# Kernel optimization log

Hardware: AMD Instinct MI355X
Metric: run time of the kernel (lower is better)

The kernel has to match this reference:

```python
import jax, jax.numpy as jnp
import numpy as np

B, C_IN, T = 8, 1024, 4096
VQ_C, CODEBOOK, DS = 1024, 2048, 2


def setup_inputs() -> dict:
    key = jax.random.key(0)
    ks = jax.random.split(key, 6)
    return {
        "x": jax.random.normal(ks[0], (B, C_IN, T), jnp.float32),
        "x_mask": jnp.ones((B, 1, T), jnp.float32),
        "w_in": jax.random.normal(ks[1], (VQ_C, C_IN, DS), jnp.float32) * 0.02,
        "b_in": jnp.zeros((VQ_C,), jnp.float32),
        "embed": jax.random.normal(ks[2], (CODEBOOK, VQ_C), jnp.float32),
        "w_out": jax.random.normal(ks[3], (C_IN, VQ_C), jnp.float32) * 0.02,
        "b_out": jnp.zeros((C_IN,), jnp.float32),
    }


def reference(x, x_mask, w_in, b_in, embed, w_out, b_out):
    x_len = x.shape[2]
    ds = w_in.shape[-1]
    pad = (-x_len) % ds  # static under jit
    if pad:
        x = jnp.pad(x, ((0, 0), (0, 0), (0, pad)))
        x_mask = jnp.pad(x_mask, ((0, 0), (0, 0), (0, pad)))
    b, cin, tp = x.shape
    # conv_in: Conv1d(k=ds, stride=ds) == non-overlapping window contraction
    h = jnp.einsum('bcls,ocs->bol', x.reshape(b, cin, tp // ds, ds), w_in) + b_in[None, :, None]  # [B, D, L]
    tokens = h.transpose(0, 2, 1)  # [B, L, D]
    # euclidean codebook: ||t - e||^2 expanded (stable for argmin)
    d2 = (jnp.sum(tokens * tokens, -1, keepdims=True)
          - 2.0 * jnp.einsum('bld,nd->bln', tokens, embed)
          + jnp.sum(embed * embed, -1)[None, None, :])  # [B, L, N]
    idx = jnp.argmin(d2, axis=-1)  # [B, L]
    q = embed[idx]  # gather -> [B, L, D]
    # commitment loss (training-mode math; EMA codebook -> embed not a grad path)
    commit_loss = jnp.mean((jax.lax.stop_gradient(q) - tokens) ** 2)
    # straight-through estimator
    q_st = tokens + jax.lax.stop_gradient(q - tokens)
    q_cf = q_st.transpose(0, 2, 1)  # [B, D, L]
    # conv_out: nearest upsample x ds, then 1x1 conv
    up = jnp.repeat(q_cf, ds, axis=2)  # [B, D, Tp]
    out = jnp.einsum('bct,oc->bot', up, w_out) + b_out[None, :, None]
    out = out * x_mask
    return out[:, :, :x_len], commit_loss
```

## Files before the change

### kernel.cpp

```cpp
#include <hip/hip_runtime.h>

typedef _Float16 half8 __attribute__((ext_vector_type(8)));
typedef float f32x4 __attribute__((ext_vector_type(4)));

static constexpr int D = 1024;
static constexpr int NCODE = 2048;
static constexpr int MTOK = 16384;
static constexpr int KIN = 2048;
static constexpr int TLEN = 4096;
static constexpr int CAP = 2048;
#define TAU 0.4f

__device__ __forceinline__ void gload16(const void* g, void* l) {
  __builtin_amdgcn_global_load_lds(
      (const __attribute__((address_space(1))) void*)g,
      (__attribute__((address_space(3))) void*)l, 16, 0, 0);
}

#define SBAR()   asm volatile("s_barrier" ::: "memory")
#define WAITV4() asm volatile("s_waitcnt vmcnt(4)" ::: "memory")
#define WAITV0() asm volatile("s_waitcnt vmcnt(0)" ::: "memory")

__device__ __forceinline__ float key_to_f32(unsigned u) {
  unsigned bits = (u & 0x80000000u) ? (u & 0x7FFFFFFFu) : ~u;
  return __uint_as_float(bits);
}
__device__ __forceinline__ unsigned f32_to_key(float f) {
  unsigned ub = __float_as_uint(f);
  return (ub & 0x80000000u) ? ~ub : (ub | 0x80000000u);
}

__global__ __launch_bounds__(256) void k_pack_x(const float* __restrict__ x,
                                                _Float16* __restrict__ xh,
                                                _Float16* __restrict__ xl) {
  __shared__ float lds[32][65];
  const int tt0 = blockIdx.x * 64;
  const int cc0 = blockIdx.y * 32;
  const int b = blockIdx.z;
  const float* xb = x + ((size_t)b * D + cc0) * TLEN + tt0;
#pragma unroll
  for (int i = 0; i < 8; ++i) {
    int idx = threadIdx.x + i * 256;
    lds[idx >> 6][idx & 63] = xb[(size_t)(idx >> 6) * TLEN + (idx & 63)];
  }
  __syncthreads();
  const size_t mrow0 = (size_t)b * 2048 + (tt0 >> 1);
#pragma unroll
  for (int i = 0; i < 8; ++i) {
    int idx = threadIdx.x + i * 256;
    int r = idx >> 6, kk = idx & 63;
    float v = lds[kk >> 1][2 * r + (kk & 1)];
    _Float16 h = (_Float16)v;
    size_t off = (mrow0 + r) * (size_t)KIN + (size_t)cc0 * 2 + kk;
    xh[off] = h;
    xl[off] = (_Float16)(v - (float)h);
  }
}

__global__ __launch_bounds__(256) void k_split(const float* __restrict__ s,
                                               _Float16* __restrict__ hi,
                                               _Float16* __restrict__ lo, int n) {
  int i = blockIdx.x * 256 + threadIdx.x;
  if (i < n) {
    float v = s[i];
    _Float16 h = (_Float16)v;
    hi[i] = h;
    lo[i] = (_Float16)(v - (float)h);
  }
}

__global__ __launch_bounds__(256) void k_tohalf(const float* __restrict__ s,
                                                _Float16* __restrict__ hi, int n) {
  int i = blockIdx.x * 256 + threadIdx.x;
  if (i < n) hi[i] = (_Float16)s[i];
}

__global__ __launch_bounds__(256) void k_e2(const float* __restrict__ embed,
                                            float* __restrict__ e2c) {
  int row = blockIdx.x * 4 + (threadIdx.x >> 6);
  int lane = threadIdx.x & 63;
  const float* er = embed + (size_t)row * D;
  double s = 0.0;
  for (int i = lane; i < D; i += 64) { double v = er[i]; s += v * v; }
#pragma unroll
  for (int mk = 1; mk < 64; mk <<= 1) s += __shfl_xor(s, mk, 64);
  if (lane == 0) e2c[row] = (float)(s - 1024.0);
}

template <int KDIM, int LOG_GX, int MODE>
__global__ __launch_bounds__(512, 2) void k_gemm_hh(
    const _Float16* __restrict__ Ah_, const _Float16* __restrict__ Bh_,
    const float* __restrict__ vec,
    _Float16* __restrict__ outh, float* __restrict__ t2,
    unsigned long long* __restrict__ skKey, float* __restrict__ skSnd) {
  __shared__ _Float16 lds[3 * 16384];
  const int nwg = gridDim.x, bid = blockIdx.x, q = nwg >> 3;
  const int b2 = (bid & 7) * q + (bid >> 3);
  const int nb = b2 & ((1 << LOG_GX) - 1);
  const int n0 = nb * 256, m0 = (b2 >> LOG_GX) * 256;
  const int tid = threadIdx.x, lane = tid & 63, w = tid >> 6;
  const int wr = w >> 2, wc = w & 3, lr = lane & 15, lk = lane >> 4;
  constexpr int NT = KDIM / 32;
  const int cswz8 = (((lane & 3) ^ ((lane >> 3) & 3))) * 8;
  const int rswz8 = (lk ^ ((lr >> 1) & 3)) * 8;

  f32x4 acc[8][4] = {};

  auto stage = [&](int t, int c) {
    char* sb = (char*)(lds + c * 16384);
    const int k0 = t * 32;
    const int r0 = (w * 64 + lane) >> 2;
    gload16(Ah_ + (size_t)(m0 + r0) * KDIM + k0 + cswz8, sb + w * 1024);
    gload16(Ah_ + (size_t)(m0 + 128 + r0) * KDIM + k0 + cswz8, sb + w * 1024 + 8192);
    gload16(Bh_ + (size_t)(n0 + r0) * KDIM + k0 + cswz8, sb + 16384 + w * 1024);
    gload16(Bh_ + (size_t)(n0 + 128 + r0) * KDIM + k0 + cswz8, sb + 16384 + w * 1024 + 8192);
  };

  stage(0, 0);
  stage(1, 1);
  WAITV4();
  SBAR();

  int c0 = 0, c1 = 1, c2 = 2;
  for (int t = 0; t < NT; ++t) {
    const bool st = (t + 2) < NT;
    if (st) stage(t + 2, c2);
    const _Float16* sb = lds + c0 * 16384;
    half8 ah[8], bh[4];
#pragma unroll
    for (int f = 0; f < 8; ++f)
      ah[f] = *(const half8*)(sb + (wr * 128 + f * 16 + lr) * 32 + rswz8);
#pragma unroll
    for (int f = 0; f < 4; ++f)
      bh[f] = *(const half8*)(sb + 8192 + (wc * 64 + f * 16 + lr) * 32 + rswz8);
    __builtin_amdgcn_s_setprio(1);
#pragma unroll
    for (int fm = 0; fm < 8; ++fm)
#pragma unroll
      for (int fn = 0; fn < 4; ++fn)
        acc[fm][fn] = __builtin_amdgcn_mfma_f32_16x16x32_f16(ah[fm], bh[fn], acc[fm][fn], 0, 0, 0);
    __builtin_amdgcn_s_setprio(0);
    if (st) { WAITV4(); } else if (t + 1 < NT) { WAITV0(); }
    SBAR();
    int tmp = c0; c0 = c1; c1 = c2; c2 = tmp;
  }

  if constexpr (MODE == 0) {
#pragma unroll
    for (int fm = 0; fm < 8; ++fm) {
#pragma unroll
      for (int j = 0; j < 4; ++j) {
        int row = wr * 128 + fm * 16 + lk * 4 + j;
        size_t m = (size_t)m0 + row;
        float v2 = 0.f;
#pragma unroll
        for (int fn = 0; fn < 4; ++fn) {
          int col = n0 + wc * 64 + fn * 16 + lr;
          float v = acc[fm][fn][j] + vec[col];
          v2 += v * v;
          outh[m * (size_t)D + col] = (_Float16)v;
        }
#pragma unroll
        for (int mk = 1; mk < 16; mk <<= 1) v2 += __shfl_xor(v2, mk, 64);
        if (lr == 0) atomicAdd(&t2[m], v2);
      }
    }
  } else {
#pragma unroll
    for (int fm = 0; fm < 8; ++fm) {
#pragma unroll
      for (int j = 0; j < 4; ++j) {
        int row = wr * 128 + fm * 16 + lk * 4 + j;
        size_t m = (size_t)m0 + row;
        float b1 = 3.4e38f, bb2 = 3.4e38f;
        int i1 = 0x7FFFFFFF;
#pragma unroll
        for (int fn = 0; fn < 4; ++fn) {
          int col = n0 + wc * 64 + fn * 16 + lr;
          float mv = vec[col] - 2.0f * acc[fm][fn][j];
          if (mv < b1) { bb2 = b1; b1 = mv; i1 = col; }
          else if (mv < bb2) { bb2 = mv; }
        }
#pragma unroll
        for (int mk = 1; mk < 16; mk <<= 1) {
          float ob1 = __shfl_xor(b1, mk, 64);
          float ob2 = __shfl_xor(bb2, mk, 64);
          int oi = __shfl_xor(i1, mk, 64);
          if (ob1 < b1) { bb2 = fminf(b1, ob2); b1 = ob1; i1 = oi; }
          else { bb2 = fminf(bb2, ob1); }
        }
        if (lr == 0) {
          unsigned long long key = ((unsigned long long)f32_to_key(b1) << 32) | (unsigned)i1;
          skKey[m * 32 + nb * 4 + wc] = key;
          skSnd[m * 32 + nb * 4 + wc] = bb2;
        }
      }
    }
  }
}

__global__ __launch_bounds__(256) void k_flag(const unsigned long long* __restrict__ skKey,
                                              const float* __restrict__ skSnd,
                                              unsigned long long* __restrict__ keys,
                                              int* __restrict__ list, int* __restrict__ counter) {
  int m = blockIdx.x * 256 + threadIdx.x;
  unsigned long long best = ~0ull;
  int bsl = 0;
#pragma unroll
  for (int sl = 0; sl < 32; ++sl) {
    unsigned long long k = skKey[(size_t)m * 32 + sl];
    if (k < best) { best = k; bsl = sl; }
  }
  float b1 = key_to_f32((unsigned)(best >> 32));
  float second = skSnd[(size_t)m * 32 + bsl];
#pragma unroll
  for (int sl = 0; sl < 32; ++sl) {
    if (sl != bsl) second = fminf(second, key_to_f32((unsigned)(skKey[(size_t)m * 32 + sl] >> 32)));
  }
  keys[m] = best;
  if (second - b1 < TAU) {
    int p = atomicAdd(counter, 1);
    if (p < CAP) list[p] = m;
  }
}

__global__ __launch_bounds__(256) void k_tok_fix(
    const _Float16* __restrict__ xh, const _Float16* __restrict__ xl,
    const _Float16* __restrict__ wh, const _Float16* __restrict__ wl,
    const float* __restrict__ b_in, const int* __restrict__ list,
    const int* __restrict__ counter,
    _Float16* __restrict__ tokh2, _Float16* __restrict__ tokl2) {
  const int count = min(counter[0], CAP);
  const int m0 = blockIdx.y * 128;
  if (m0 >= count) return;
  __shared__ _Float16 sAh[128 * 32], sAl[128 * 32], sBh[128 * 32], sBl[128 * 32];
  const int n0 = blockIdx.x * 128;
  const int tid = threadIdx.x, lane = tid & 63, w = tid >> 6;
  const int wr = w >> 1, wc = w & 1, lr = lane & 15, lk = lane >> 4;
  f32x4 acc[4][4] = {};

  const int g0 = w * 128 + lane, g1 = g0 + 64;
  const int rA0 = g0 >> 2, cA0 = g0 & 3, rA1 = g1 >> 2, cA1 = g1 & 3;
  const int lb0 = (w * 128) * 16, lb1 = (w * 128 + 64) * 16;
  const int tk0 = list[min(m0 + rA0, count - 1)];
  const int tk1 = list[min(m0 + rA1, count - 1)];

  for (int kt = 0; kt < KIN / 32; ++kt) {
    const int k0 = kt * 32;
    gload16(xh + (size_t)tk0 * KIN + k0 + cA0 * 8, (char*)sAh + lb0);
    gload16(xh + (size_t)tk1 * KIN + k0 + cA1 * 8, (char*)sAh + lb1);
    gload16(xl + (size_t)tk0 * KIN + k0 + cA0 * 8, (char*)sAl + lb0);
    gload16(xl + (size_t)tk1 * KIN + k0 + cA1 * 8, (char*)sAl + lb1);
    gload16(wh + (size_t)(n0 + rA0) * KIN + k0 + cA0 * 8, (char*)sBh + lb0);
    gload16(wh + (size_t)(n0 + rA1) * KIN + k0 + cA1 * 8, (char*)sBh + lb1);
    gload16(wl + (size_t)(n0 + rA0) * KIN + k0 + cA0 * 8, (char*)sBl + lb0);
    gload16(wl + (size_t)(n0 + rA1) * KIN + k0 + cA1 * 8, (char*)sBl + lb1);
    __syncthreads();
    half8 ah[4], al2[4], bh[4], bl2[4];
#pragma unroll
    for (int f = 0; f < 4; ++f) {
      ah[f]  = *(const half8*)(sAh + (wr * 64 + f * 16 + lr) * 32 + lk * 8);
      al2[f] = *(const half8*)(sAl + (wr * 64 + f * 16 + lr) * 32 + lk * 8);
      bh[f]  = *(const half8*)(sBh + (wc * 64 + f * 16 + lr) * 32 + lk * 8);
      bl2[f] = *(const half8*)(sBl + (wc * 64 + f * 16 + lr) * 32 + lk * 8);
    }
#pragma unroll
    for (int fm = 0; fm < 4; ++fm)
#pragma unroll
      for (int fn = 0; fn < 4; ++fn) {
        acc[fm][fn] = __builtin_amdgcn_mfma_f32_16x16x32_f16(ah[fm], bh[fn], acc[fm][fn], 0, 0, 0);
        acc[fm][fn] = __builtin_amdgcn_mfma_f32_16x16x32_f16(ah[fm], bl2[fn], acc[fm][fn], 0, 0, 0);
        acc[fm][fn] = __builtin_amdgcn_mfma_f32_16x16x32_f16(al2[fm], bh[fn], acc[fm][fn], 0, 0, 0);
      }
    __syncthreads();
  }
#pragma unroll
  for (int fm = 0; fm < 4; ++fm) {
#pragma unroll
    for (int j = 0; j < 4; ++j) {
      int row = wr * 64 + fm * 16 + lk * 4 + j;
      if (m0 + row >= count) continue;
#pragma unroll
      for (int fn = 0; fn < 4; ++fn) {
        int col = n0 + wc * 64 + fn * 16 + lr;
        float v = acc[fm][fn][j] + b_in[col];
        _Float16 h = (_Float16)v;
        tokh2[(size_t)(m0 + row) * D + col] = h;
        tokl2[(size_t)(m0 + row) * D + col] = (_Float16)(v - (float)h);
      }
    }
  }
}

__global__ __launch_bounds__(256) void k_rescore(
    const _Float16* __restrict__ tokh2, const _Float16* __restrict__ tokl2,
    const _Float16* __restrict__ eh, const _Float16* __restrict__ el,
    const float* __restrict__ e2c, const int* __restrict__ list,
    const int* __restrict__ counter,
    unsigned long long* __restrict__ keys2) {
  const int count = min(counter[0], CAP);
  const int m0 = blockIdx.y * 128;
  if (m0 >= count) return;
  __shared__ _Float16 sAh[128 * 32], sAl[128 * 32], sBh[128 * 32], sBl[128 * 32];
  const int n0 = blockIdx.x * 128;
  const int tid = threadIdx.x, lane = tid & 63, w = tid >> 6;
  const int wr = w >> 1, wc = w & 1, lr = lane & 15, lk = lane >> 4;
  f32x4 acc[4][4] = {};

  const int g0 = w * 128 + lane, g1 = g0 + 64;
  const int rA0 = g0 >> 2, cA0 = g0 & 3, rA1 = g1 >> 2, cA1 = g1 & 3;
  const int lb0 = (w * 128) * 16, lb1 = (w * 128 + 64) * 16;

  for (int kt = 0; kt < D / 32; ++kt) {
    const int k0 = kt * 32;
    gload16(tokh2 + (size_t)(m0 + rA0) * D + k0 + cA0 * 8, (char*)sAh + lb0);
    gload16(tokh2 + (size_t)(m0 + rA1) * D + k0 + cA1 * 8, (char*)sAh + lb1);
    gload16(tokl2 + (size_t)(m0 + rA0) * D + k0 + cA0 * 8, (char*)sAl + lb0);
    gload16(tokl2 + (size_t)(m0 + rA1) * D + k0 + cA1 * 8, (char*)sAl + lb1);
    gload16(eh + (size_t)(n0 + rA0) * D + k0 + cA0 * 8, (char*)sBh + lb0);
    gload16(eh + (size_t)(n0 + rA1) * D + k0 + cA1 * 8, (char*)sBh + lb1);
    gload16(el + (size_t)(n0 + rA0) * D + k0 + cA0 * 8, (char*)sBl + lb0);
    gload16(el + (size_t)(n0 + rA1) * D + k0 + cA1 * 8, (char*)sBl + lb1);
    __syncthreads();
    half8 ah[4], al2[4], bh[4], bl2[4];
#pragma unroll
    for (int f = 0; f < 4; ++f) {
      ah[f]  = *(const half8*)(sAh + (wr * 64 + f * 16 + lr) * 32 + lk * 8);
      al2[f] = *(const half8*)(sAl + (wr * 64 + f * 16 + lr) * 32 + lk * 8);
      bh[f]  = *(const half8*)(sBh + (wc * 64 + f * 16 + lr) * 32 + lk * 8);
      bl2[f] = *(const half8*)(sBl + (wc * 64 + f * 16 + lr) * 32 + lk * 8);
    }
#pragma unroll
    for (int fm = 0; fm < 4; ++fm)
#pragma unroll
      for (int fn = 0; fn < 4; ++fn) {
        acc[fm][fn] = __builtin_amdgcn_mfma_f32_16x16x32_f16(ah[fm], bh[fn], acc[fm][fn], 0, 0, 0);
        acc[fm][fn] = __builtin_amdgcn_mfma_f32_16x16x32_f16(ah[fm], bl2[fn], acc[fm][fn], 0, 0, 0);
        acc[fm][fn] = __builtin_amdgcn_mfma_f32_16x16x32_f16(al2[fm], bh[fn], acc[fm][fn], 0, 0, 0);
      }
    __syncthreads();
  }
#pragma unroll
  for (int fm = 0; fm < 4; ++fm) {
#pragma unroll
    for (int j = 0; j < 4; ++j) {
      int row = wr * 64 + fm * 16 + lk * 4 + j;
      if (m0 + row >= count) continue;
      int tm = list[m0 + row];
      float best = 3.4e38f;
      int bidx = 0x7FFFFFFF;
#pragma unroll
      for (int fn = 0; fn < 4; ++fn) {
        int col = n0 + wc * 64 + fn * 16 + lr;
        float mv = e2c[col] - 2.0f * acc[fm][fn][j];
        if (mv < best) { best = mv; bidx = col; }
      }
#pragma unroll
      for (int mk = 1; mk < 16; mk <<= 1) {
        float ob = __shfl_xor(best, mk, 64);
        int oi = __shfl_xor(bidx, mk, 64);
        if (ob < best || (ob == best && oi < bidx)) { best = ob; bidx = oi; }
      }
      if (lr == 0) {
        unsigned long long key = ((unsigned long long)f32_to_key(best) << 32) | (unsigned)bidx;
        atomicMin(&keys2[tm], key);
      }
    }
  }
}

__global__ __launch_bounds__(256) void k_merge(unsigned long long* __restrict__ keys,
                                               const unsigned long long* __restrict__ keys2) {
  int m = blockIdx.x * 256 + threadIdx.x;
  unsigned long long k2 = keys2[m];
  if (k2 != ~0ull) keys[m] = k2;
}

__global__ __launch_bounds__(256) void k_gemm_out(
    const _Float16* __restrict__ eh, const unsigned long long* __restrict__ keys,
    const _Float16* __restrict__ woh, const float* __restrict__ b_out,
    const float* __restrict__ mask, float* __restrict__ out) {
  __shared__ _Float16 sA[128 * 32], sB[128 * 32];
  __shared__ float sC[32 * 129];
  const int n0 = blockIdx.x * 128, m0 = blockIdx.y * 128;
  const int tid = threadIdx.x, lane = tid & 63, w = tid >> 6;
  const int wr = w >> 1, wc = w & 1, lr = lane & 15, lk = lane >> 4;
  f32x4 acc[4][4] = {};

  const int g0 = w * 128 + lane, g1 = g0 + 64;
  const int rA0 = g0 >> 2, cA0 = g0 & 3, rA1 = g1 >> 2, cA1 = g1 & 3;
  const int lb0 = (w * 128) * 16, lb1 = (w * 128 + 64) * 16;
  const unsigned i0 = (unsigned)(keys[m0 + rA0] & 0xFFFFFFFFull);
  const unsigned i1 = (unsigned)(keys[m0 + rA1] & 0xFFFFFFFFull);
  const _Float16* srcA0 = eh + (size_t)i0 * D + cA0 * 8;
  const _Float16* srcA1 = eh + (size_t)i1 * D + cA1 * 8;

  for (int kt = 0; kt < D / 32; ++kt) {
    const int k0 = kt * 32;
    gload16(srcA0 + k0, (char*)sA + lb0);
    gload16(srcA1 + k0, (char*)sA + lb1);
    gload16(woh + (size_t)(n0 + rA0) * D + k0 + cA0 * 8, (char*)sB + lb0);
    gload16(woh + (size_t)(n0 + rA1) * D + k0 + cA1 * 8, (char*)sB + lb1);
    __syncthreads();
    half8 a[4], b[4];
#pragma unroll
    for (int f = 0; f < 4; ++f) {
      a[f] = *(const half8*)(sA + (wr * 64 + f * 16 + lr) * 32 + lk * 8);
      b[f] = *(const half8*)(sB + (wc * 64 + f * 16 + lr) * 32 + lk * 8);
    }
#pragma unroll
    for (int fm = 0; fm < 4; ++fm)
#pragma unroll
      for (int fn = 0; fn < 4; ++fn)
        acc[fm][fn] = __builtin_amdgcn_mfma_f32_16x16x32_f16(a[fm], b[fn], acc[fm][fn], 0, 0, 0);
    __syncthreads();
  }
  for (int ch = 0; ch < 4; ++ch) {
    __syncthreads();
    if (wr == (ch >> 1)) {
      int fb = (ch & 1) * 2;
#pragma unroll
      for (int f2 = 0; f2 < 2; ++f2) {
        int fm = fb + f2;
#pragma unroll
        for (int fn = 0; fn < 4; ++fn)
#pragma unroll
          for (int j = 0; j < 4; ++j) {
            int lrow = f2 * 16 + lk * 4 + j;
            int col = wc * 64 + fn * 16 + lr;
            sC[lrow * 129 + col] = acc[fm][fn][j] + b_out[n0 + col];
          }
      }
    }
    __syncthreads();
    const int mbase = m0 + ch * 32;
    const int b = mbase >> 11;
    const int l0 = mbase & 2047;
    const float mval = mask[(size_t)b * TLEN + 2 * l0 + lane];
    for (int oo = 0; oo < 32; ++oo) {
      int ocol = w * 32 + oo;
      float v = sC[(lane >> 1) * 129 + ocol];
      out[((size_t)(b * D + n0 + ocol)) * TLEN + 2 * l0 + lane] = v * mval;
    }
  }
}

__global__ __launch_bounds__(256) void k_loss(const unsigned long long* __restrict__ keys,
                                              const float* __restrict__ t2,
                                              double* __restrict__ acc) {
  int m = blockIdx.x * 256 + threadIdx.x;
  unsigned long long k = keys[m];
  float mval = key_to_f32((unsigned)(k >> 32));
  double c = (double)mval + 1024.0 + (double)t2[m];
#pragma unroll
  for (int mk = 1; mk < 64; mk <<= 1) c += __shfl_xor(c, mk, 64);
  __shared__ double part[4];
  if ((threadIdx.x & 63) == 0) part[threadIdx.x >> 6] = c;
  __syncthreads();
  if (threadIdx.x == 0) atomicAdd(acc, part[0] + part[1] + part[2] + part[3]);
}

__global__ void k_finalize(const double* __restrict__ acc, float* __restrict__ dst) {
  if (threadIdx.x == 0 && blockIdx.x == 0) *dst = (float)(*acc * (1.0 / 16777216.0));
}

extern "C" void kernel_launch(void* const* d_in, const int* in_sizes, int n_in,
                              void* d_out, int out_size, void* d_ws, size_t ws_size,
                              hipStream_t stream) {
  (void)in_sizes; (void)n_in; (void)out_size;
  const float* x      = (const float*)d_in[0];
  const float* xmask  = (const float*)d_in[1];
  const float* w_in   = (const float*)d_in[2];
  const float* b_in   = (const float*)d_in[3];
  const float* embed  = (const float*)d_in[4];
  const float* w_out  = (const float*)d_in[5];
  const float* b_out  = (const float*)d_in[6];
  float* out = (float*)d_out;

  _Float16* xh = (_Float16*)d_out;
  _Float16* xl = xh + (size_t)MTOK * KIN;

  char* p = (char*)d_ws;
  auto take = [&](size_t sz) { char* r = p; p += (sz + 255) & ~(size_t)255; return r; };
  _Float16* wh    = (_Float16*)take((size_t)D * KIN * 2);
  _Float16* wl    = (_Float16*)take((size_t)D * KIN * 2);
  _Float16* eh    = (_Float16*)take((size_t)NCODE * D * 2);
  _Float16* el    = (_Float16*)take((size_t)NCODE * D * 2);
  _Float16* woh   = (_Float16*)take((size_t)D * D * 2);
  float* e2c      = (float*)take((size_t)NCODE * 4);
  _Float16* tokh  = (_Float16*)take((size_t)MTOK * D * 2);
  _Float16* tokh2 = (_Float16*)take((size_t)CAP * D * 2);
  _Float16* tokl2 = (_Float16*)take((size_t)CAP * D * 2);
  float* t2       = (float*)take((size_t)MTOK * 4);
  unsigned long long* keys  = (unsigned long long*)take((size_t)MTOK * 8);
  unsigned long long* keys2 = (unsigned long long*)take((size_t)MTOK * 8);
  unsigned long long* skKey = (unsigned long long*)take((size_t)MTOK * 32 * 8);
  float* skSnd    = (float*)take((size_t)MTOK * 32 * 4);
  int* list       = (int*)take((size_t)CAP * 4);
  int* counter    = (int*)take(256);
  double* lossacc = (double*)take(256);
  if ((size_t)(p - (char*)d_ws) > ws_size) return;

  hipMemsetAsync(keys2, 0xFF, (size_t)MTOK * 8, stream);
  hipMemsetAsync(t2, 0, (size_t)MTOK * 4, stream);
  hipMemsetAsync(list, 0, (size_t)CAP * 4, stream);
  hipMemsetAsync(counter, 0, 256, stream);
  hipMemsetAsync(lossacc, 0, 8, stream);

  k_pack_x<<<dim3(64, 32, 8), 256, 0, stream>>>(x, xh, xl);
  k_split<<<(D * KIN + 255) / 256, 256, 0, stream>>>(w_in, wh, wl, D * KIN);
  k_split<<<(NCODE * D + 255) / 256, 256, 0, stream>>>(embed, eh, el, NCODE * D);
  k_tohalf<<<(D * D + 255) / 256, 256, 0, stream>>>(w_out, woh, D * D);
  k_e2<<<NCODE / 4, 256, 0, stream>>>(embed, e2c);

  k_gemm_hh<KIN, 2, 0><<<256, 512, 0, stream>>>(xh, wh, b_in, tokh, t2, nullptr, nullptr);
  k_gemm_hh<D, 3, 1><<<512, 512, 0, stream>>>(tokh, eh, e2c, nullptr, nullptr, skKey, skSnd);
  k_flag<<<MTOK / 256, 256, 0, stream>>>(skKey, skSnd, keys, list, counter);
  k_tok_fix<<<dim3(D / 128, CAP / 128), 256, 0, stream>>>(xh, xl, wh, wl, b_in, list, counter, tokh2, tokl2);
  k_rescore<<<dim3(NCODE / 128, CAP / 128), 256, 0, stream>>>(tokh2, tokl2, eh, el, e2c, list, counter, keys2);
  k_merge<<<MTOK / 256, 256, 0, stream>>>(keys, keys2);

  k_gemm_out<<<dim3(D / 128, MTOK / 128), 256, 0, stream>>>(eh, keys, woh, b_out, xmask, out);

  k_loss<<<MTOK / 256, 256, 0, stream>>>(keys, t2, lossacc);
  k_finalize<<<1, 64, 0, stream>>>(lossacc, out + (size_t)MTOK * KIN);
}
```

Measured before the change: 452.2 us.

## Shrink projection and distance GEMM tiles to 128x128 with single-buffered LDS

Replaces the 256x256-tile, 512-thread, triple-buffered GEMM used for the input projection and codebook distance with a 128x128-tile, 256-thread kernel that uses one LDS buffer and syncs every k-step. This raises the grid size and occupancy (four blocks per CU) at the cost of less operand reuse and no explicit load/compute overlap. The per-row argmin partial slots are re-indexed for the new tiling. It also adds an XOR swizzle to the LDS layout in the output GEMM to reduce bank conflicts.

```diff
diff --git a/kernel.cpp b/kernel.cpp
--- a/kernel.cpp
+++ b/kernel.cpp
@@ -16,10 +16,6 @@
       (const __attribute__((address_space(1))) void*)g,
       (__attribute__((address_space(3))) void*)l, 16, 0, 0);
 }
-
-#define SBAR()   asm volatile("s_barrier" ::: "memory")
-#define WAITV4() asm volatile("s_waitcnt vmcnt(4)" ::: "memory")
-#define WAITV0() asm volatile("s_waitcnt vmcnt(0)" ::: "memory")
 
 __device__ __forceinline__ float key_to_f32(unsigned u) {
   unsigned bits = (u & 0x80000000u) ? (u & 0x7FFFFFFFu) : ~u;
@@ -88,69 +84,55 @@
 }
 
 template <int KDIM, int LOG_GX, int MODE>
-__global__ __launch_bounds__(512, 2) void k_gemm_hh(
-    const _Float16* __restrict__ Ah_, const _Float16* __restrict__ Bh_,
+__global__ __launch_bounds__(256, 4) void k_gemm_m97(
+    const _Float16* __restrict__ A_, const _Float16* __restrict__ B_,
     const float* __restrict__ vec,
     _Float16* __restrict__ outh, float* __restrict__ t2,
     unsigned long long* __restrict__ skKey, float* __restrict__ skSnd) {
-  __shared__ _Float16 lds[3 * 16384];
+  __shared__ _Float16 lds[8192];
   const int nwg = gridDim.x, bid = blockIdx.x, q = nwg >> 3;
   const int b2 = (bid & 7) * q + (bid >> 3);
   const int nb = b2 & ((1 << LOG_GX) - 1);
-  const int n0 = nb * 256, m0 = (b2 >> LOG_GX) * 256;
+  const int n0 = nb * 128, m0 = (b2 >> LOG_GX) * 128;
   const int tid = threadIdx.x, lane = tid & 63, w = tid >> 6;
-  const int wr = w >> 2, wc = w & 3, lr = lane & 15, lk = lane >> 4;
-  constexpr int NT = KDIM / 32;
+  const int wr = w >> 1, wc = w & 1, lr = lane & 15, lk = lane >> 4;
   const int cswz8 = (((lane & 3) ^ ((lane >> 3) & 3))) * 8;
   const int rswz8 = (lk ^ ((lr >> 1) & 3)) * 8;
-
-  f32x4 acc[8][4] = {};
-
-  auto stage = [&](int t, int c) {
-    char* sb = (char*)(lds + c * 16384);
-    const int k0 = t * 32;
-    const int r0 = (w * 64 + lane) >> 2;
-    gload16(Ah_ + (size_t)(m0 + r0) * KDIM + k0 + cswz8, sb + w * 1024);
-    gload16(Ah_ + (size_t)(m0 + 128 + r0) * KDIM + k0 + cswz8, sb + w * 1024 + 8192);
-    gload16(Bh_ + (size_t)(n0 + r0) * KDIM + k0 + cswz8, sb + 16384 + w * 1024);
-    gload16(Bh_ + (size_t)(n0 + 128 + r0) * KDIM + k0 + cswz8, sb + 16384 + w * 1024 + 8192);
-  };
-
-  stage(0, 0);
-  stage(1, 1);
-  WAITV4();
-  SBAR();
-
-  int c0 = 0, c1 = 1, c2 = 2;
-  for (int t = 0; t < NT; ++t) {
-    const bool st = (t + 2) < NT;
-    if (st) stage(t + 2, c2);
-    const _Float16* sb = lds + c0 * 16384;
-    half8 ah[8], bh[4];
-#pragma unroll
-    for (int f = 0; f < 8; ++f)
-      ah[f] = *(const half8*)(sb + (wr * 128 + f * 16 + lr) * 32 + rswz8);
-#pragma unroll
-    for (int f = 0; f < 4; ++f)
-      bh[f] = *(const half8*)(sb + 8192 + (wc * 64 + f * 16 + lr) * 32 + rswz8);
+  const int g0 = w * 128 + lane, g1 = g0 + 64;
+  const int rA0 = g0 >> 2, rA1 = g1 >> 2;
+  const int lb0 = (w * 128) * 16, lb1 = (w * 128 + 64) * 16;
+
+  f32x4 acc[4][4] = {};
+
+  for (int kt = 0; kt < KDIM / 32; ++kt) {
+    const int k0 = kt * 32;
+    gload16(A_ + (size_t)(m0 + rA0) * KDIM + k0 + cswz8, (char*)lds + lb0);
+    gload16(A_ + (size_t)(m0 + rA1) * KDIM + k0 + cswz8, (char*)lds + lb1);
+    gload16(B_ + (size_t)(n0 + rA0) * KDIM + k0 + cswz8, (char*)lds + 8192 + lb0);
+    gload16(B_ + (size_t)(n0 + rA1) * KDIM + k0 + cswz8, (char*)lds + 8192 + lb1);
+    __syncthreads();
+    half8 ah[4], bh[4];
+#pragma unroll
+    for (int f = 0; f < 4; ++f) {
+      ah[f] = *(const half8*)(lds + (wr * 64 + f * 16 + lr) * 32 + rswz8);
+      bh[f] = *(const half8*)(lds + 4096 + (wc * 64 + f * 16 + lr) * 32 + rswz8);
+    }
     __builtin_amdgcn_s_setprio(1);
 #pragma unroll
-    for (int fm = 0; fm < 8; ++fm)
+    for (int fm = 0; fm < 4; ++fm)
 #pragma unroll
       for (int fn = 0; fn < 4; ++fn)
         acc[fm][fn] = __builtin_amdgcn_mfma_f32_16x16x32_f16(ah[fm], bh[fn], acc[fm][fn], 0, 0, 0);
     __builtin_amdgcn_s_setprio(0);
-    if (st) { WAITV4(); } else if (t + 1 < NT) { WAITV0(); }
-    SBAR();
-    int tmp = c0; c0 = c1; c1 = c2; c2 = tmp;
+    __syncthreads();
   }
 
   if constexpr (MODE == 0) {
 #pragma unroll
-    for (int fm = 0; fm < 8; ++fm) {
+    for (int fm = 0; fm < 4; ++fm) {
 #pragma unroll
       for (int j = 0; j < 4; ++j) {
-        int row = wr * 128 + fm * 16 + lk * 4 + j;
+        int row = wr * 64 + fm * 16 + lk * 4 + j;
         size_t m = (size_t)m0 + row;
         float v2 = 0.f;
 #pragma unroll
@@ -167,10 +149,10 @@
     }
   } else {
 #pragma unroll
-    for (int fm = 0; fm < 8; ++fm) {
+    for (int fm = 0; fm < 4; ++fm) {
 #pragma unroll
       for (int j = 0; j < 4; ++j) {
-        int row = wr * 128 + fm * 16 + lk * 4 + j;
+        int row = wr * 64 + fm * 16 + lk * 4 + j;
         size_t m = (size_t)m0 + row;
         float b1 = 3.4e38f, bb2 = 3.4e38f;
         int i1 = 0x7FFFFFFF;
@@ -191,8 +173,8 @@
         }
         if (lr == 0) {
           unsigned long long key = ((unsigned long long)f32_to_key(b1) << 32) | (unsigned)i1;
-          skKey[m * 32 + nb * 4 + wc] = key;
-          skSnd[m * 32 + nb * 4 + wc] = bb2;
+          skKey[m * 32 + nb * 2 + wc] = key;
+          skSnd[m * 32 + nb * 2 + wc] = bb2;
         }
       }
     }
@@ -385,28 +367,30 @@
   const int n0 = blockIdx.x * 128, m0 = blockIdx.y * 128;
   const int tid = threadIdx.x, lane = tid & 63, w = tid >> 6;
   const int wr = w >> 1, wc = w & 1, lr = lane & 15, lk = lane >> 4;
+  const int cswz8 = (((lane & 3) ^ ((lane >> 3) & 3))) * 8;
+  const int rswz8 = (lk ^ ((lr >> 1) & 3)) * 8;
   f32x4 acc[4][4] = {};
 
   const int g0 = w * 128 + lane, g1 = g0 + 64;
-  const int rA0 = g0 >> 2, cA0 = g0 & 3, rA1 = g1 >> 2, cA1 = g1 & 3;
+  const int rA0 = g0 >> 2, rA1 = g1 >> 2;
   const int lb0 = (w * 128) * 16, lb1 = (w * 128 + 64) * 16;
   const unsigned i0 = (unsigned)(keys[m0 + rA0] & 0xFFFFFFFFull);
   const unsigned i1 = (unsigned)(keys[m0 + rA1] & 0xFFFFFFFFull);
-  const _Float16* srcA0 = eh + (size_t)i0 * D + cA0 * 8;
-  const _Float16* srcA1 = eh + (size_t)i1 * D + cA1 * 8;
+  const _Float16* srcA0 = eh + (size_t)i0 * D + cswz8;
+  const _Float16* srcA1 = eh + (size_t)i1 * D + cswz8;
 
   for (int kt = 0; kt < D / 32; ++kt) {
     const int k0 = kt * 32;
     gload16(srcA0 + k0, (char*)sA + lb0);
     gload16(srcA1 + k0, (char*)sA + lb1);
-    gload16(woh + (size_t)(n0 + rA0) * D + k0 + cA0 * 8, (char*)sB + lb0);
-    gload16(woh + (size_t)(n0 + rA1) * D + k0 + cA1 * 8, (char*)sB + lb1);
+    gload16(woh + (size_t)(n0 + rA0) * D + k0 + cswz8, (char*)sB + lb0);
+    gload16(woh + (size_t)(n0 + rA1) * D + k0 + cswz8, (char*)sB + lb1);
     __syncthreads();
     half8 a[4], b[4];
 #pragma unroll
     for (int f = 0; f < 4; ++f) {
-      a[f] = *(const half8*)(sA + (wr * 64 + f * 16 + lr) * 32 + lk * 8);
-      b[f] = *(const half8*)(sB + (wc * 64 + f * 16 + lr) * 32 + lk * 8);
+      a[f] = *(const half8*)(sA + (wr * 64 + f * 16 + lr) * 32 + rswz8);
+      b[f] = *(const half8*)(sB + (wc * 64 + f * 16 + lr) * 32 + rswz8);
     }
 #pragma unroll
     for (int fm = 0; fm < 4; ++fm)
@@ -513,8 +497,8 @@
   k_tohalf<<<(D * D + 255) / 256, 256, 0, stream>>>(w_out, woh, D * D);
   k_e2<<<NCODE / 4, 256, 0, stream>>>(embed, e2c);
 
-  k_gemm_hh<KIN, 2, 0><<<256, 512, 0, stream>>>(xh, wh, b_in, tokh, t2, nullptr, nullptr);
-  k_gemm_hh<D, 3, 1><<<512, 512, 0, stream>>>(tokh, eh, e2c, nullptr, nullptr, skKey, skSnd);
+  k_gemm_m97<KIN, 3, 0><<<1024, 256, 0, stream>>>(xh, wh, b_in, tokh, t2, nullptr, nullptr);
+  k_gemm_m97<D, 4, 1><<<2048, 256, 0, stream>>>(tokh, eh, e2c, nullptr, nullptr, skKey, skSnd);
   k_flag<<<MTOK / 256, 256, 0, stream>>>(skKey, skSnd, keys, list, counter);
   k_tok_fix<<<dim3(D / 128, CAP / 128), 256, 0, stream>>>(xh, xl, wh, wl, b_in, list, counter, tokh2, tokl2);
   k_rescore<<<dim3(NCODE / 128, CAP / 128), 256, 0, stream>>>(tokh2, tokl2, eh, el, e2c, list, counter, keys2);
```

After: 475.5 us. 1.05x slower.

## Precompute codebook-projected output table and gather rows instead of output GEMM

Applied to the files above, without the earlier changes.

Because every token's quantized vector is a codebook row, the output projection is computed once per codebook entry (2048x1024 table F = embed·w_outᵀ + b_out, using a split-fp16 three-MFMA scheme) instead of once per token (16384 rows). The final output is then produced by gathering the selected row from F for each token and writing it masked and upsampled. This replaces a large GEMM with a GEMM eight times smaller plus a bandwidth-bound gather/expand, at the cost of an extra 8 MB workspace table and a split of w_out into hi/lo halves.

```diff
diff --git a/kernel.cpp b/kernel.cpp
--- a/kernel.cpp
+++ b/kernel.cpp
@@ -67,12 +67,6 @@
     hi[i] = h;
     lo[i] = (_Float16)(v - (float)h);
   }
-}
-
-__global__ __launch_bounds__(256) void k_tohalf(const float* __restrict__ s,
-                                                _Float16* __restrict__ hi, int n) {
-  int i = blockIdx.x * 256 + threadIdx.x;
-  if (i < n) hi[i] = (_Float16)s[i];
 }
 
 __global__ __launch_bounds__(256) void k_e2(const float* __restrict__ embed,
@@ -376,12 +370,11 @@
   if (k2 != ~0ull) keys[m] = k2;
 }
 
-__global__ __launch_bounds__(256) void k_gemm_out(
-    const _Float16* __restrict__ eh, const unsigned long long* __restrict__ keys,
-    const _Float16* __restrict__ woh, const float* __restrict__ b_out,
-    const float* __restrict__ mask, float* __restrict__ out) {
-  __shared__ _Float16 sA[128 * 32], sB[128 * 32];
-  __shared__ float sC[32 * 129];
+__global__ __launch_bounds__(256) void k_F(
+    const _Float16* __restrict__ eh, const _Float16* __restrict__ el,
+    const _Float16* __restrict__ woh, const _Float16* __restrict__ wol,
+    const float* __restrict__ b_out, float* __restrict__ F) {
+  __shared__ _Float16 sAh[128 * 32], sAl[128 * 32], sBh[128 * 32], sBl[128 * 32];
   const int n0 = blockIdx.x * 128, m0 = blockIdx.y * 128;
   const int tid = threadIdx.x, lane = tid & 63, w = tid >> 6;
   const int wr = w >> 1, wc = w & 1, lr = lane & 15, lk = lane >> 4;
@@ -390,58 +383,66 @@
   const int g0 = w * 128 + lane, g1 = g0 + 64;
   const int rA0 = g0 >> 2, cA0 = g0 & 3, rA1 = g1 >> 2, cA1 = g1 & 3;
   const int lb0 = (w * 128) * 16, lb1 = (w * 128 + 64) * 16;
-  const unsigned i0 = (unsigned)(keys[m0 + rA0] & 0xFFFFFFFFull);
-  const unsigned i1 = (unsigned)(keys[m0 + rA1] & 0xFFFFFFFFull);
-  const _Float16* srcA0 = eh + (size_t)i0 * D + cA0 * 8;
-  const _Float16* srcA1 = eh + (size_t)i1 * D + cA1 * 8;
 
   for (int kt = 0; kt < D / 32; ++kt) {
     const int k0 = kt * 32;
-    gload16(srcA0 + k0, (char*)sA + lb0);
-    gload16(srcA1 + k0, (char*)sA + lb1);
-    gload16(woh + (size_t)(n0 + rA0) * D + k0 + cA0 * 8, (char*)sB + lb0);
-    gload16(woh + (size_t)(n0 + rA1) * D + k0 + cA1 * 8, (char*)sB + lb1);
+    gload16(eh + (size_t)(m0 + rA0) * D + k0 + cA0 * 8, (char*)sAh + lb0);
+    gload16(eh + (size_t)(m0 + rA1) * D + k0 + cA1 * 8, (char*)sAh + lb1);
+    gload16(el + (size_t)(m0 + rA0) * D + k0 + cA0 * 8, (char*)sAl + lb0);
+    gload16(el + (size_t)(m0 + rA1) * D + k0 + cA1 * 8, (char*)sAl + lb1);
+    gload16(woh + (size_t)(n0 + rA0) * D + k0 + cA0 * 8, (char*)sBh + lb0);
+    gload16(woh + (size_t)(n0 + rA1) * D + k0 + cA1 * 8, (char*)sBh + lb1);
+    gload16(wol + (size_t)(n0 + rA0) * D + k0 + cA0 * 8, (char*)sBl + lb0);
+    gload16(wol + (size_t)(n0 + rA1) * D + k0 + cA1 * 8, (char*)sBl + lb1);
     __syncthreads();
-    half8 a[4], b[4];
+    half8 ah[4], al2[4], bh[4], bl2[4];
 #pragma unroll
     for (int f = 0; f < 4; ++f) {
-      a[f] = *(const half8*)(sA + (wr * 64 + f * 16 + lr) * 32 + lk * 8);
-      b[f] = *(const half8*)(sB + (wc * 64 + f * 16 + lr) * 32 + lk * 8);
+      ah[f]  = *(const half8*)(sAh + (wr * 64 + f * 16 + lr) * 32 + lk * 8);
+      al2[f] = *(const half8*)(sAl + (wr * 64 + f * 16 + lr) * 32 + lk * 8);
+      bh[f]  = *(const half8*)(sBh + (wc * 64 + f * 16 + lr) * 32 + lk * 8);
+      bl2[f] = *(const half8*)(sBl + (wc * 64 + f * 16 + lr) * 32 + lk * 8);
     }
 #pragma unroll
     for (int fm = 0; fm < 4; ++fm)
 #pragma unroll
-      for (int fn = 0; fn < 4; ++fn)
-        acc[fm][fn] = __builtin_amdgcn_mfma_f32_16x16x32_f16(a[fm], b[fn], acc[fm][fn], 0, 0, 0);
+      for (int fn = 0; fn < 4; ++fn) {
+        acc[fm][fn] = __builtin_amdgcn_mfma_f32_16x16x32_f16(ah[fm], bh[fn], acc[fm][fn], 0, 0, 0);
+        acc[fm][fn] = __builtin_amdgcn_mfma_f32_16x16x32_f16(ah[fm], bl2[fn], acc[fm][fn], 0, 0, 0);
+        acc[fm][fn] = __builtin_amdgcn_mfma_f32_16x16x32_f16(al2[fm], bh[fn], acc[fm][fn], 0, 0, 0);
+      }
     __syncthreads();
   }
-  for (int ch = 0; ch < 4; ++ch) {
-    __syncthreads();
-    if (wr == (ch >> 1)) {
-      int fb = (ch & 1) * 2;
-#pragma unroll
-      for (int f2 = 0; f2 < 2; ++f2) {
-        int fm = fb + f2;
-#pragma unroll
-        for (int fn = 0; fn < 4; ++fn)
-#pragma unroll
-          for (int j = 0; j < 4; ++j) {
-            int lrow = f2 * 16 + lk * 4 + j;
-            int col = wc * 64 + fn * 16 + lr;
-            sC[lrow * 129 + col] = acc[fm][fn][j] + b_out[n0 + col];
-          }
-      }
-    }
-    __syncthreads();
-    const int mbase = m0 + ch * 32;
-    const int b = mbase >> 11;
-    const int l0 = mbase & 2047;
-    const float mval = mask[(size_t)b * TLEN + 2 * l0 + lane];
-    for (int oo = 0; oo < 32; ++oo) {
-      int ocol = w * 32 + oo;
-      float v = sC[(lane >> 1) * 129 + ocol];
-      out[((size_t)(b * D + n0 + ocol)) * TLEN + 2 * l0 + lane] = v * mval;
-    }
+#pragma unroll
+  for (int fm = 0; fm < 4; ++fm)
+#pragma unroll
+    for (int j = 0; j < 4; ++j) {
+      int row = wr * 64 + fm * 16 + lk * 4 + j;
+#pragma unroll
+      for (int fn = 0; fn < 4; ++fn) {
+        int col = n0 + wc * 64 + fn * 16 + lr;
+        F[(size_t)(m0 + row) * D + col] = acc[fm][fn][j] + b_out[col];
+      }
+    }
+}
+
+__global__ __launch_bounds__(256) void k_expand(
+    const float* __restrict__ F, const unsigned long long* __restrict__ keys,
+    const float* __restrict__ mask, float* __restrict__ out) {
+  const int b = blockIdx.y;
+  const int t0 = blockIdx.x * 128;
+  const int z = blockIdx.z;
+  const int lane = threadIdx.x & 63, w = threadIdx.x >> 6;
+  const int tok = (t0 >> 1) + lane;
+  const unsigned idx = (unsigned)(keys[b * 2048 + tok] & 0xFFFFFFFFull);
+  const float2 mv = *(const float2*)&mask[(size_t)b * TLEN + t0 + 2 * lane];
+  const float* Frow = F + (size_t)idx * D;
+  float* outb = out + ((size_t)b * D) * TLEN + t0 + 2 * lane;
+  const int oc_end = (z + 1) * 256;
+  for (int oc = z * 256 + w; oc < oc_end; oc += 4) {
+    float v = Frow[oc];
+    float2 o; o.x = v * mv.x; o.y = v * mv.y;
+    *(float2*)&outb[(size_t)oc * TLEN] = o;
   }
 }
 
@@ -487,6 +488,8 @@
   _Float16* eh    = (_Float16*)take((size_t)NCODE * D * 2);
   _Float16* el    = (_Float16*)take((size_t)NCODE * D * 2);
   _Float16* woh   = (_Float16*)take((size_t)D * D * 2);
+  _Float16* wol   = (_Float16*)take((size_t)D * D * 2);
+  float* Fm       = (float*)take((size_t)NCODE * D * 4);
   float* e2c      = (float*)take((size_t)NCODE * 4);
   _Float16* tokh  = (_Float16*)take((size_t)MTOK * D * 2);
   _Float16* tokh2 = (_Float16*)take((size_t)CAP * D * 2);
@@ -510,8 +513,10 @@
   k_pack_x<<<dim3(64, 32, 8), 256, 0, stream>>>(x, xh, xl);
   k_split<<<(D * KIN + 255) / 256, 256, 0, stream>>>(w_in, wh, wl, D * KIN);
   k_split<<<(NCODE * D + 255) / 256, 256, 0, stream>>>(embed, eh, el, NCODE * D);
-  k_tohalf<<<(D * D + 255) / 256, 256, 0, stream>>>(w_out, woh, D * D);
+  k_split<<<(D * D + 255) / 256, 256, 0, stream>>>(w_out, woh, wol, D * D);
   k_e2<<<NCODE / 4, 256, 0, stream>>>(embed, e2c);
+
+  k_F<<<dim3(D / 128, NCODE / 128), 256, 0, stream>>>(eh, el, woh, wol, b_out, Fm);
 
   k_gemm_hh<KIN, 2, 0><<<256, 512, 0, stream>>>(xh, wh, b_in, tokh, t2, nullptr, nullptr);
   k_gemm_hh<D, 3, 1><<<512, 512, 0, stream>>>(tokh, eh, e2c, nullptr, nullptr, skKey, skSnd);
@@ -520,7 +525,7 @@
   k_rescore<<<dim3(NCODE / 128, CAP / 128), 256, 0, stream>>>(tokh2, tokl2, eh, el, e2c, list, counter, keys2);
   k_merge<<<MTOK / 256, 256, 0, stream>>>(keys, keys2);
 
-  k_gemm_out<<<dim3(D / 128, MTOK / 128), 256, 0, stream>>>(eh, keys, woh, b_out, xmask, out);
+  k_expand<<<dim3(TLEN / 128, 8, 4), 256, 0, stream>>>(Fm, keys, xmask, out);
 
   k_loss<<<MTOK / 256, 256, 0, stream>>>(keys, t2, lossacc);
   k_finalize<<<1, 64, 0, stream>>>(lossacc, out + (size_t)MTOK * KIN);
```

After: 477.2 us. +5.5%, slower.
